# Kernel optimization log

Measured on AMD Instinct MI355X. Metric: run time of the kernel, lower is better.

Reference implementation:

```python
import jax, jax.numpy as jnp
import numpy as np

H = 768  # bert-base hidden size; match MLP width = 2*H = 1536


def setup_inputs() -> dict:
    key = jax.random.key(0)
    ks = jax.random.split(key, 6)
    B, S = 2, 256
    std = 0.02  # TruncatedNormal(stddev=initializer_range)
    return {
        "hidden": jax.random.normal(ks[0], (B, S, H), dtype=jnp.float32),
        "w_start": jax.random.normal(ks[1], (H, 1), dtype=jnp.float32) * std,
        "b_start": jnp.zeros((1,), jnp.float32),
        "w_end": jax.random.normal(ks[2], (H, 1), dtype=jnp.float32) * std,
        "b_end": jnp.zeros((1,), jnp.float32),
        "w1": jax.random.normal(ks[3], (2 * H, 2 * H), dtype=jnp.float32) * std,
        "b1": jnp.zeros((2 * H,), jnp.float32),
        "w2": jax.random.normal(ks[4], (2 * H, 1), dtype=jnp.float32) * std,
        "b2": jnp.zeros((1,), jnp.float32),
    }


def reference(hidden, w_start, b_start, w_end, b_end, w1, b1, w2, b2):
    # hidden: [B, S, H] = BERT sequence output (dropout disabled at inference)
    start_logits = hidden @ w_start + b_start  # [B, S, 1]
    end_logits = hidden @ w_end + b_end        # [B, S, 1]

    # Pairwise span features: concat(row_i, col_j) along last dim, fed to dense1.
    # concat([row, col]) @ w1 == row @ w1[:H] + col @ w1[H:], so we split w1 and
    # broadcast-add instead of materializing the [B,S,S,2H] concat tile.
    row_proj = hidden @ w1[:H]   # [B, S, 2H] (start-token contribution)
    col_proj = hidden @ w1[H:]   # [B, S, 2H] (end-token contribution)
    pre = row_proj[:, :, None, :] + col_proj[:, None, :, :] + b1  # [B, S, S, 2H]
    act = jax.nn.gelu(pre, approximate=False)  # keras 'gelu' is exact
    match_logits = act @ w2 + b2  # [B, S, S, 1]
    return start_logits, end_logits, match_logits
```

## Files before the change

kernel.cpp:

```cpp
#include <hip/hip_runtime.h>
#include <stdint.h>

typedef __attribute__((ext_vector_type(8))) __bf16 bf16x8;
typedef __attribute__((ext_vector_type(4))) float  floatx4;
typedef __attribute__((ext_vector_type(4))) unsigned int uint4v;
typedef __attribute__((ext_vector_type(2))) unsigned int uint2v;
typedef __attribute__((ext_vector_type(4))) float  float4v;
typedef __attribute__((ext_vector_type(2))) float  float2v;

__device__ __forceinline__ unsigned short f2bf(float f) {
  union { float f; unsigned int u; } x; x.f = f;
  unsigned int r = x.u + 0x7fffu + ((x.u >> 16) & 1u);
  return (unsigned short)(r >> 16);
}

__global__ __launch_bounds__(256) void logits_init_kernel(
    const float* __restrict__ hidden, const float* __restrict__ w_start,
    const float* __restrict__ b_start, const float* __restrict__ w_end,
    const float* __restrict__ b_end, const float* __restrict__ b2,
    float* __restrict__ out) {
  if (blockIdx.x >= 32) {
    float v = b2[0];
    int idx = ((blockIdx.x - 32) * 256 + threadIdx.x) * 4;
    *(float4v*)(out + 1024 + idx) = float4v{v, v, v, v};
    return;
  }
  const int tid  = threadIdx.x;
  const int lane = tid & 63;
  const int wv   = tid >> 6;
  const int wg   = blockIdx.x * 4 + wv;

  float wsv[12], wev[12];
#pragma unroll
  for (int t = 0; t < 12; ++t) {
    wsv[t] = w_start[lane + 64 * t];
    wev[t] = w_end[lane + 64 * t];
  }
  const float bs = b_start[0];
  const float be = b_end[0];

#pragma unroll
  for (int r = 0; r < 4; ++r) {
    int row = wg * 4 + r;
    const float* h = hidden + (size_t)row * 768;
    float ps = 0.f, pe = 0.f;
#pragma unroll
    for (int t = 0; t < 12; ++t) {
      float hv = h[lane + 64 * t];
      ps += hv * wsv[t];
      pe += hv * wev[t];
    }
#pragma unroll
    for (int off = 32; off >= 1; off >>= 1) {
      ps += __shfl_xor(ps, off, 64);
      pe += __shfl_xor(pe, off, 64);
    }
    if (lane == 0) { out[row] = ps + bs; out[512 + row] = pe + be; }
  }
}

__global__ __launch_bounds__(256) void proj_kernel(
    const float* __restrict__ hidden, const float* __restrict__ w1,
    const float* __restrict__ b1, unsigned short* __restrict__ wsR,
    unsigned short* __restrict__ wsC) {
  __shared__ short As[4 * 32 * 8];
  __shared__ short Bs[4 * 64 * 8];

  const int tid  = threadIdx.x;
  const int lane = tid & 63;
  const int wave = tid >> 6;
  const int wr = wave >> 1, wc = wave & 1;
  const int m0 = blockIdx.y * 32;
  const int n0g = blockIdx.x * 64;
  const bool isR = (n0g < 1536);
  const int kbase = isR ? 0 : 768;
  const int n0 = isR ? n0g : (n0g - 1536);
  const int q = lane >> 4, l15 = lane & 15;

  floatx4 acc0 = {}, acc1 = {};

  const int a_row = tid >> 3;
  const int a_s   = tid & 7;
  const int b_n   = tid & 63;
  const int b_kg  = tid >> 6;

  const float* hrow = hidden + (size_t)(m0 + a_row) * 768 + a_s * 4;
  const float* bcol = w1 + (size_t)(kbase + b_kg * 8) * 1536 + n0 + b_n;

  float4v hv = *(const float4v*)(hrow);
  float bv[8];
#pragma unroll
  for (int a = 0; a < 8; ++a) bv[a] = bcol[(size_t)a * 1536];

  const int aq = a_s >> 1;
  const int aj = (a_s & 1) * 4;

  for (int ko = 0; ko < 768; ko += 32) {
    uint2v au;
    au[0] = (unsigned int)f2bf(hv[0]) | ((unsigned int)f2bf(hv[1]) << 16);
    au[1] = (unsigned int)f2bf(hv[2]) | ((unsigned int)f2bf(hv[3]) << 16);
    *(uint2v*)(&As[(aq * 32 + a_row) * 8 + aj]) = au;
    uint4v pv;
#pragma unroll
    for (int a = 0; a < 4; ++a) {
      unsigned int lo = f2bf(bv[2 * a]);
      unsigned int hi = f2bf(bv[2 * a + 1]);
      pv[a] = lo | (hi << 16);
    }
    *(uint4v*)(&Bs[(b_kg * 64 + b_n) * 8]) = pv;
    __syncthreads();

    if (ko + 32 < 768) {
      hv = *(const float4v*)(hrow + ko + 32);
      const float* bp = bcol + (size_t)(ko + 32) * 1536;
#pragma unroll
      for (int a = 0; a < 8; ++a) bv[a] = bp[(size_t)a * 1536];
    }

    bf16x8 af  = *(const bf16x8*)(&As[(q * 32 + 16 * wr + l15) * 8]);
    bf16x8 bg0 = *(const bf16x8*)(&Bs[(q * 64 + 32 * wc + l15) * 8]);
    bf16x8 bg1 = *(const bf16x8*)(&Bs[(q * 64 + 32 * wc + 16 + l15) * 8]);
    acc0 = __builtin_amdgcn_mfma_f32_16x16x32_bf16(af, bg0, acc0, 0, 0, 0);
    acc1 = __builtin_amdgcn_mfma_f32_16x16x32_bf16(af, bg1, acc1, 0, 0, 0);
    __syncthreads();
  }

  unsigned short* outp = isR ? wsR : wsC;
#pragma unroll
  for (int ni = 0; ni < 2; ++ni) {
    const floatx4& ac = ni ? acc1 : acc0;
    int col = n0 + 32 * wc + 16 * ni + l15;
    float bias = isR ? b1[col] : 0.0f;
#pragma unroll
    for (int r = 0; r < 4; ++r) {
      int rowg = m0 + 16 * wr + q * 4 + r;
      outp[(size_t)rowg * 1536 + col] = f2bf(ac[r] + bias);
    }
  }
}

__device__ __forceinline__ float2v gelu2_acc(float2v x, float2v wv, float2v acc) {
  constexpr float C0 = 0.39103831f;
  constexpr float C1 = -0.05415410f;
  constexpr float C2 = 0.00461682f;
  constexpr float C3 = -1.51033e-4f;
  float2v xc;
  xc[0] = __builtin_amdgcn_fmed3f(x[0], -3.5f, 3.5f);
  xc[1] = __builtin_amdgcn_fmed3f(x[1], -3.5f, 3.5f);
  float2v u = xc * xc;
  float2v p = __builtin_elementwise_fma(u,
      __builtin_elementwise_fma(u,
          __builtin_elementwise_fma(u, float2v{C3, C3}, float2v{C2, C2}),
          float2v{C1, C1}),
      float2v{C0, C0});
  float2v t = __builtin_elementwise_fma(xc, p, float2v{0.5f, 0.5f});
  float2v g = x * t;
  return __builtin_elementwise_fma(g, wv, acc);
}

__device__ __forceinline__ void g8(float2v& acc, float4v r0, float4v r1,
                                   float4v c0, float4v c1,
                                   float4v w0, float4v w1) {
  acc = gelu2_acc(float2v{r0[0], r0[1]} + float2v{c0[0], c0[1]},
                  float2v{w0[0], w0[1]}, acc);
  acc = gelu2_acc(float2v{r0[2], r0[3]} + float2v{c0[2], c0[3]},
                  float2v{w0[2], w0[3]}, acc);
  acc = gelu2_acc(float2v{r1[0], r1[1]} + float2v{c1[0], c1[1]},
                  float2v{w1[0], w1[1]}, acc);
  acc = gelu2_acc(float2v{r1[2], r1[3]} + float2v{c1[2], c1[3]},
                  float2v{w1[2], w1[3]}, acc);
}

__device__ __forceinline__ void cvt8(uint4v v, float4v& lo4, float4v& hi4) {
  union { unsigned int u; float f; } t;
  float4v L, H;
  t.u = v[0] << 16;          L[0] = t.f;
  t.u = v[0] & 0xffff0000u;  L[1] = t.f;
  t.u = v[1] << 16;          L[2] = t.f;
  t.u = v[1] & 0xffff0000u;  L[3] = t.f;
  t.u = v[2] << 16;          H[0] = t.f;
  t.u = v[2] & 0xffff0000u;  H[1] = t.f;
  t.u = v[3] << 16;          H[2] = t.f;
  t.u = v[3] & 0xffff0000u;  H[3] = t.f;
  lo4 = L; hi4 = H;
}

__global__ __launch_bounds__(256) void match_kernel(
    const unsigned short* __restrict__ wsR,
    const unsigned short* __restrict__ wsC,
    const float* __restrict__ w2,
    float* __restrict__ outm) {
  __shared__ float Rs[32 * 132];
  __shared__ float Cs[64 * 132];
  __shared__ float Ws[128];

  const int tid = threadIdx.x;
  const int jt = blockIdx.x;
  const int it = blockIdx.y;
  const int bz = blockIdx.z >> 2;
  const int kh = blockIdx.z & 3;

  const int rg  = tid >> 4;
  const int cgl = tid & 15;

  float2v accA0 = {}, accA1 = {}, accA2 = {}, accA3 = {};
  float2v accB0 = {}, accB1 = {}, accB2 = {}, accB3 = {};

  const int srow = tid >> 4;
  const int sseg = tid & 15;

  const float* rp0 = &Rs[(2 * rg + 0) * 132];
  const float* rp1 = &Rs[(2 * rg + 1) * 132];
  const float* cp0 = &Cs[(cgl +  0) * 132];
  const float* cp1 = &Cs[(cgl + 16) * 132];
  const float* cp2 = &Cs[(cgl + 32) * 132];
  const float* cp3 = &Cs[(cgl + 48) * 132];

  for (int kc = 0; kc < 3; ++kc) {
    const int Kb = kh * 384 + kc * 128;
#pragma unroll
    for (int a = 0; a < 2; ++a) {
      int row = srow + 16 * a;
      const unsigned short* g =
          wsR + (size_t)(bz * 256 + it * 32 + row) * 1536 + Kb + sseg * 8;
      uint4v v = *(const uint4v*)g;
      float4v lo, hi; cvt8(v, lo, hi);
      float* d = &Rs[row * 132 + sseg * 8];
      *(float4v*)d = lo;
      *(float4v*)(d + 4) = hi;
    }
#pragma unroll
    for (int a = 0; a < 4; ++a) {
      int row = srow + 16 * a;
      const unsigned short* g =
          wsC + (size_t)(bz * 256 + jt * 64 + row) * 1536 + Kb + sseg * 8;
      uint4v v = *(const uint4v*)g;
      float4v lo, hi; cvt8(v, lo, hi);
      float* d = &Cs[row * 132 + sseg * 8];
      *(float4v*)d = lo;
      *(float4v*)(d + 4) = hi;
    }
    if (tid < 128) Ws[tid] = w2[Kb + tid];
    __syncthreads();

#pragma unroll 2
    for (int k = 0; k < 128; k += 8) {
      float4v ra0 = *(const float4v*)(rp0 + k);
      float4v ra1 = *(const float4v*)(rp0 + k + 4);
      float4v rb0 = *(const float4v*)(rp1 + k);
      float4v rb1 = *(const float4v*)(rp1 + k + 4);
      float4v w0  = *(const float4v*)(&Ws[k]);
      float4v w1  = *(const float4v*)(&Ws[k + 4]);
      {
        float4v c0 = *(const float4v*)(cp0 + k);
        float4v c1 = *(const float4v*)(cp0 + k + 4);
        g8(accA0, ra0, ra1, c0, c1, w0, w1);
        g8(accB0, rb0, rb1, c0, c1, w0, w1);
      }
      {
        float4v c0 = *(const float4v*)(cp1 + k);
        float4v c1 = *(const float4v*)(cp1 + k + 4);
        g8(accA1, ra0, ra1, c0, c1, w0, w1);
        g8(accB1, rb0, rb1, c0, c1, w0, w1);
      }
      {
        float4v c0 = *(const float4v*)(cp2 + k);
        float4v c1 = *(const float4v*)(cp2 + k + 4);
        g8(accA2, ra0, ra1, c0, c1, w0, w1);
        g8(accB2, rb0, rb1, c0, c1, w0, w1);
      }
      {
        float4v c0 = *(const float4v*)(cp3 + k);
        float4v c1 = *(const float4v*)(cp3 + k + 4);
        g8(accA3, ra0, ra1, c0, c1, w0, w1);
        g8(accB3, rb0, rb1, c0, c1, w0, w1);
      }
    }
    __syncthreads();
  }

  const size_t rowA = (size_t)(bz * 256 + it * 32 + 2 * rg);
  const size_t base = rowA * 256 + jt * 64 + cgl;
  unsafeAtomicAdd(&outm[base +  0], accA0[0] + accA0[1]);
  unsafeAtomicAdd(&outm[base + 16], accA1[0] + accA1[1]);
  unsafeAtomicAdd(&outm[base + 32], accA2[0] + accA2[1]);
  unsafeAtomicAdd(&outm[base + 48], accA3[0] + accA3[1]);
  unsafeAtomicAdd(&outm[base + 256 +  0], accB0[0] + accB0[1]);
  unsafeAtomicAdd(&outm[base + 256 + 16], accB1[0] + accB1[1]);
  unsafeAtomicAdd(&outm[base + 256 + 32], accB2[0] + accB2[1]);
  unsafeAtomicAdd(&outm[base + 256 + 48], accB3[0] + accB3[1]);
}

extern "C" void kernel_launch(void* const* d_in, const int* in_sizes, int n_in,
                              void* d_out, int out_size, void* d_ws, size_t ws_size,
                              hipStream_t stream) {
  const float* hidden  = (const float*)d_in[0];
  const float* w_start = (const float*)d_in[1];
  const float* b_start = (const float*)d_in[2];
  const float* w_end   = (const float*)d_in[3];
  const float* b_end   = (const float*)d_in[4];
  const float* w1      = (const float*)d_in[5];
  const float* b1      = (const float*)d_in[6];
  const float* w2      = (const float*)d_in[7];
  const float* b2      = (const float*)d_in[8];

  float* out = (float*)d_out;
  char* ws = (char*)d_ws;
  unsigned short* wsR = (unsigned short*)(ws);
  unsigned short* wsC = (unsigned short*)(ws + 1572864);

  logits_init_kernel<<<dim3(160), dim3(256), 0, stream>>>(
      hidden, w_start, b_start, w_end, b_end, b2, out);
  proj_kernel<<<dim3(48, 16), dim3(256), 0, stream>>>(hidden, w1, b1, wsR, wsC);
  match_kernel<<<dim3(4, 8, 8), dim3(256), 0, stream>>>(wsR, wsC, w2, out + 1024);
}
```

Measured before the change: 147.3 us.

## Split match kernel K across more blocks and force packed f32 GELU ops

Doubles the K-split of the match kernel from 4 to 8 slices (grid z 8→16), halving each block's K chunk to 64 and shrinking shared tiles. This doubles the block count (256→512) for better occupancy and smaller LDS per block. It also replaces vector-builtin GELU arithmetic with inline-asm v_pk_add/mul/fma_f32 so two lanes are processed per instruction. The cost is more atomic/partial writes to the output and inline asm that may hinder compiler scheduling.

```diff
diff --git a/kernel.cpp b/kernel.cpp
--- a/kernel.cpp
+++ b/kernel.cpp
@@ -139,36 +139,51 @@
   }
 }
 
-__device__ __forceinline__ float2v gelu2_acc(float2v x, float2v wv, float2v acc) {
-  constexpr float C0 = 0.39103831f;
-  constexpr float C1 = -0.05415410f;
-  constexpr float C2 = 0.00461682f;
-  constexpr float C3 = -1.51033e-4f;
+__device__ __forceinline__ float2v pk_add(float2v a, float2v b) {
+  float2v d;
+  asm("v_pk_add_f32 %0, %1, %2" : "=v"(d) : "v"(a), "v"(b));
+  return d;
+}
+__device__ __forceinline__ float2v pk_mul(float2v a, float2v b) {
+  float2v d;
+  asm("v_pk_mul_f32 %0, %1, %2" : "=v"(d) : "v"(a), "v"(b));
+  return d;
+}
+__device__ __forceinline__ float2v pk_fma(float2v a, float2v b, float2v c) {
+  float2v d;
+  asm("v_pk_fma_f32 %0, %1, %2, %3" : "=v"(d) : "v"(a), "v"(b), "v"(c));
+  return d;
+}
+
+__device__ __forceinline__ void gelu2_acc(float2v& acc, float2v r, float2v c,
+                                          float2v wv) {
+  const float2v C0v = {0.39103831f, 0.39103831f};
+  const float2v C1v = {-0.05415410f, -0.05415410f};
+  const float2v C2v = {0.00461682f, 0.00461682f};
+  const float2v C3v = {-1.51033e-4f, -1.51033e-4f};
+  const float2v H = {0.5f, 0.5f};
+  float2v x = pk_add(r, c);
   float2v xc;
   xc[0] = __builtin_amdgcn_fmed3f(x[0], -3.5f, 3.5f);
   xc[1] = __builtin_amdgcn_fmed3f(x[1], -3.5f, 3.5f);
-  float2v u = xc * xc;
-  float2v p = __builtin_elementwise_fma(u,
-      __builtin_elementwise_fma(u,
-          __builtin_elementwise_fma(u, float2v{C3, C3}, float2v{C2, C2}),
-          float2v{C1, C1}),
-      float2v{C0, C0});
-  float2v t = __builtin_elementwise_fma(xc, p, float2v{0.5f, 0.5f});
-  float2v g = x * t;
-  return __builtin_elementwise_fma(g, wv, acc);
+  float2v u = pk_mul(xc, xc);
+  float2v p = pk_fma(u, pk_fma(u, pk_fma(u, C3v, C2v), C1v), C0v);
+  float2v t = pk_fma(xc, p, H);
+  float2v g = pk_mul(x, t);
+  acc = pk_fma(g, wv, acc);
 }
 
 __device__ __forceinline__ void g8(float2v& acc, float4v r0, float4v r1,
                                    float4v c0, float4v c1,
                                    float4v w0, float4v w1) {
-  acc = gelu2_acc(float2v{r0[0], r0[1]} + float2v{c0[0], c0[1]},
-                  float2v{w0[0], w0[1]}, acc);
-  acc = gelu2_acc(float2v{r0[2], r0[3]} + float2v{c0[2], c0[3]},
-                  float2v{w0[2], w0[3]}, acc);
-  acc = gelu2_acc(float2v{r1[0], r1[1]} + float2v{c1[0], c1[1]},
-                  float2v{w1[0], w1[1]}, acc);
-  acc = gelu2_acc(float2v{r1[2], r1[3]} + float2v{c1[2], c1[3]},
-                  float2v{w1[2], w1[3]}, acc);
+  gelu2_acc(acc, float2v{r0[0], r0[1]}, float2v{c0[0], c0[1]},
+            float2v{w0[0], w0[1]});
+  gelu2_acc(acc, float2v{r0[2], r0[3]}, float2v{c0[2], c0[3]},
+            float2v{w0[2], w0[3]});
+  gelu2_acc(acc, float2v{r1[0], r1[1]}, float2v{c1[0], c1[1]},
+            float2v{w1[0], w1[1]});
+  gelu2_acc(acc, float2v{r1[2], r1[3]}, float2v{c1[2], c1[3]},
+            float2v{w1[2], w1[3]});
 }
 
 __device__ __forceinline__ void cvt8(uint4v v, float4v& lo4, float4v& hi4) {
@@ -190,15 +205,15 @@
     const unsigned short* __restrict__ wsC,
     const float* __restrict__ w2,
     float* __restrict__ outm) {
-  __shared__ float Rs[32 * 132];
-  __shared__ float Cs[64 * 132];
-  __shared__ float Ws[128];
+  __shared__ float Rs[32 * 68];
+  __shared__ float Cs[64 * 68];
+  __shared__ float Ws[64];
 
   const int tid = threadIdx.x;
   const int jt = blockIdx.x;
   const int it = blockIdx.y;
-  const int bz = blockIdx.z >> 2;
-  const int kh = blockIdx.z & 3;
+  const int bz = blockIdx.z >> 3;
+  const int kh = blockIdx.z & 7;
 
   const int rg  = tid >> 4;
   const int cgl = tid & 15;
@@ -206,45 +221,43 @@
   float2v accA0 = {}, accA1 = {}, accA2 = {}, accA3 = {};
   float2v accB0 = {}, accB1 = {}, accB2 = {}, accB3 = {};
 
-  const int srow = tid >> 4;
-  const int sseg = tid & 15;
-
-  const float* rp0 = &Rs[(2 * rg + 0) * 132];
-  const float* rp1 = &Rs[(2 * rg + 1) * 132];
-  const float* cp0 = &Cs[(cgl +  0) * 132];
-  const float* cp1 = &Cs[(cgl + 16) * 132];
-  const float* cp2 = &Cs[(cgl + 32) * 132];
-  const float* cp3 = &Cs[(cgl + 48) * 132];
+  const int srow = tid >> 3;
+  const int sseg = tid & 7;
+
+  const float* rp0 = &Rs[(2 * rg + 0) * 68];
+  const float* rp1 = &Rs[(2 * rg + 1) * 68];
+  const float* cp0 = &Cs[(cgl +  0) * 68];
+  const float* cp1 = &Cs[(cgl + 16) * 68];
+  const float* cp2 = &Cs[(cgl + 32) * 68];
+  const float* cp3 = &Cs[(cgl + 48) * 68];
 
   for (int kc = 0; kc < 3; ++kc) {
-    const int Kb = kh * 384 + kc * 128;
-#pragma unroll
-    for (int a = 0; a < 2; ++a) {
-      int row = srow + 16 * a;
+    const int Kb = kh * 192 + kc * 64;
+    {
       const unsigned short* g =
-          wsR + (size_t)(bz * 256 + it * 32 + row) * 1536 + Kb + sseg * 8;
+          wsR + (size_t)(bz * 256 + it * 32 + srow) * 1536 + Kb + sseg * 8;
       uint4v v = *(const uint4v*)g;
       float4v lo, hi; cvt8(v, lo, hi);
-      float* d = &Rs[row * 132 + sseg * 8];
+      float* d = &Rs[srow * 68 + sseg * 8];
       *(float4v*)d = lo;
       *(float4v*)(d + 4) = hi;
     }
 #pragma unroll
-    for (int a = 0; a < 4; ++a) {
-      int row = srow + 16 * a;
+    for (int a = 0; a < 2; ++a) {
+      int row = srow + 32 * a;
       const unsigned short* g =
           wsC + (size_t)(bz * 256 + jt * 64 + row) * 1536 + Kb + sseg * 8;
       uint4v v = *(const uint4v*)g;
       float4v lo, hi; cvt8(v, lo, hi);
-      float* d = &Cs[row * 132 + sseg * 8];
+      float* d = &Cs[row * 68 + sseg * 8];
       *(float4v*)d = lo;
       *(float4v*)(d + 4) = hi;
     }
-    if (tid < 128) Ws[tid] = w2[Kb + tid];
+    if (tid < 64) Ws[tid] = w2[Kb + tid];
     __syncthreads();
 
 #pragma unroll 2
-    for (int k = 0; k < 128; k += 8) {
+    for (int k = 0; k < 64; k += 8) {
       float4v ra0 = *(const float4v*)(rp0 + k);
       float4v ra1 = *(const float4v*)(rp0 + k + 4);
       float4v rb0 = *(const float4v*)(rp1 + k);
@@ -312,5 +325,5 @@
   logits_init_kernel<<<dim3(160), dim3(256), 0, stream>>>(
       hidden, w_start, b_start, w_end, b_end, b2, out);
   proj_kernel<<<dim3(48, 16), dim3(256), 0, stream>>>(hidden, w1, b1, wsR, wsC);
-  match_kernel<<<dim3(4, 8, 8), dim3(256), 0, stream>>>(wsR, wsC, w2, out + 1024);
-}
+  match_kernel<<<dim3(4, 8, 16), dim3(256), 0, stream>>>(wsR, wsC, w2, out + 1024);
+}
```

After: 131.5 us. 1.12x faster.

## Evaluate GELU in packed fp16 with fdot2 and fuse logits into projection

Applied to the files above, without the earlier changes.

Converts the bf16 projections to packed fp16 in shared memory and evaluates the polynomial GELU with half2 arithmetic. Each weighted pair is accumulated with fdot2, which roughly doubles ALU throughput per instruction in the dominant match kernel. The K dimension is split 24 ways instead of 4, so there are more blocks and more atomics. The start/end logits and the output initialisation are folded into an extra row of the projection grid, removing one launch. The fp16 polynomial carries accuracy risk relative to the exact GELU.

```diff
diff --git a/kernel.cpp b/kernel.cpp
--- a/kernel.cpp
+++ b/kernel.cpp
@@ -6,7 +6,7 @@
 typedef __attribute__((ext_vector_type(4))) unsigned int uint4v;
 typedef __attribute__((ext_vector_type(2))) unsigned int uint2v;
 typedef __attribute__((ext_vector_type(4))) float  float4v;
-typedef __attribute__((ext_vector_type(2))) float  float2v;
+typedef __attribute__((ext_vector_type(2))) _Float16 half2v;
 
 __device__ __forceinline__ unsigned short f2bf(float f) {
   union { float f; unsigned int u; } x; x.f = f;
@@ -14,59 +14,59 @@
   return (unsigned short)(r >> 16);
 }
 
-__global__ __launch_bounds__(256) void logits_init_kernel(
-    const float* __restrict__ hidden, const float* __restrict__ w_start,
-    const float* __restrict__ b_start, const float* __restrict__ w_end,
-    const float* __restrict__ b_end, const float* __restrict__ b2,
-    float* __restrict__ out) {
-  if (blockIdx.x >= 32) {
-    float v = b2[0];
-    int idx = ((blockIdx.x - 32) * 256 + threadIdx.x) * 4;
-    *(float4v*)(out + 1024 + idx) = float4v{v, v, v, v};
-    return;
-  }
-  const int tid  = threadIdx.x;
-  const int lane = tid & 63;
-  const int wv   = tid >> 6;
-  const int wg   = blockIdx.x * 4 + wv;
-
-  float wsv[12], wev[12];
-#pragma unroll
-  for (int t = 0; t < 12; ++t) {
-    wsv[t] = w_start[lane + 64 * t];
-    wev[t] = w_end[lane + 64 * t];
-  }
-  const float bs = b_start[0];
-  const float be = b_end[0];
-
-#pragma unroll
-  for (int r = 0; r < 4; ++r) {
-    int row = wg * 4 + r;
-    const float* h = hidden + (size_t)row * 768;
-    float ps = 0.f, pe = 0.f;
-#pragma unroll
-    for (int t = 0; t < 12; ++t) {
-      float hv = h[lane + 64 * t];
-      ps += hv * wsv[t];
-      pe += hv * wev[t];
-    }
-#pragma unroll
-    for (int off = 32; off >= 1; off >>= 1) {
-      ps += __shfl_xor(ps, off, 64);
-      pe += __shfl_xor(pe, off, 64);
-    }
-    if (lane == 0) { out[row] = ps + bs; out[512 + row] = pe + be; }
-  }
-}
-
 __global__ __launch_bounds__(256) void proj_kernel(
     const float* __restrict__ hidden, const float* __restrict__ w1,
     const float* __restrict__ b1, unsigned short* __restrict__ wsR,
-    unsigned short* __restrict__ wsC) {
+    unsigned short* __restrict__ wsC,
+    const float* __restrict__ w_start, const float* __restrict__ b_start,
+    const float* __restrict__ w_end, const float* __restrict__ b_end,
+    const float* __restrict__ b2, float* __restrict__ out) {
+  const int tid  = threadIdx.x;
+  if (blockIdx.y == 16) {
+    if (blockIdx.x >= 32) {
+      float v = b2[0];
+      float4v vv = {v, v, v, v};
+      int base = (blockIdx.x - 32) * 8192 + tid * 4;
+#pragma unroll
+      for (int itr = 0; itr < 8; ++itr)
+        *(float4v*)(out + 1024 + base + itr * 1024) = vv;
+      return;
+    }
+    const int lane = tid & 63;
+    const int wv   = tid >> 6;
+    const int wg   = blockIdx.x * 4 + wv;
+    float wsv[12], wev[12];
+#pragma unroll
+    for (int t = 0; t < 12; ++t) {
+      wsv[t] = w_start[lane + 64 * t];
+      wev[t] = w_end[lane + 64 * t];
+    }
+    const float bs = b_start[0];
+    const float be = b_end[0];
+#pragma unroll
+    for (int r = 0; r < 4; ++r) {
+      int row = wg * 4 + r;
+      const float* h = hidden + (size_t)row * 768;
+      float ps = 0.f, pe = 0.f;
+#pragma unroll
+      for (int t = 0; t < 12; ++t) {
+        float hv = h[lane + 64 * t];
+        ps += hv * wsv[t];
+        pe += hv * wev[t];
+      }
+#pragma unroll
+      for (int off = 32; off >= 1; off >>= 1) {
+        ps += __shfl_xor(ps, off, 64);
+        pe += __shfl_xor(pe, off, 64);
+      }
+      if (lane == 0) { out[row] = ps + bs; out[512 + row] = pe + be; }
+    }
+    return;
+  }
+
   __shared__ short As[4 * 32 * 8];
   __shared__ short Bs[4 * 64 * 8];
 
-  const int tid  = threadIdx.x;
   const int lane = tid & 63;
   const int wave = tid >> 6;
   const int wr = wave >> 1, wc = wave & 1;
@@ -139,50 +139,41 @@
   }
 }
 
-__device__ __forceinline__ float2v gelu2_acc(float2v x, float2v wv, float2v acc) {
-  constexpr float C0 = 0.39103831f;
-  constexpr float C1 = -0.05415410f;
-  constexpr float C2 = 0.00461682f;
-  constexpr float C3 = -1.51033e-4f;
-  float2v xc;
-  xc[0] = __builtin_amdgcn_fmed3f(x[0], -3.5f, 3.5f);
-  xc[1] = __builtin_amdgcn_fmed3f(x[1], -3.5f, 3.5f);
-  float2v u = xc * xc;
-  float2v p = __builtin_elementwise_fma(u,
+__device__ __forceinline__ void gelu_pair(float& acc, unsigned int ru,
+                                          unsigned int cu, unsigned int wu) {
+  const half2v C3 = {(_Float16)-1.51033e-4f, (_Float16)-1.51033e-4f};
+  const half2v C2 = {(_Float16)0.00461682f, (_Float16)0.00461682f};
+  const half2v C1 = {(_Float16)-0.05415410f, (_Float16)-0.05415410f};
+  const half2v C0 = {(_Float16)0.39103831f, (_Float16)0.39103831f};
+  const half2v HI = {(_Float16)3.5f, (_Float16)3.5f};
+  const half2v LO = {(_Float16)-3.5f, (_Float16)-3.5f};
+  const half2v HALF = {(_Float16)0.5f, (_Float16)0.5f};
+  half2v r = __builtin_bit_cast(half2v, ru);
+  half2v c = __builtin_bit_cast(half2v, cu);
+  half2v w = __builtin_bit_cast(half2v, wu);
+  half2v x = r + c;
+  half2v xc = __builtin_elementwise_min(
+      __builtin_elementwise_max(x, LO), HI);
+  half2v u = xc * xc;
+  half2v p = __builtin_elementwise_fma(u,
       __builtin_elementwise_fma(u,
-          __builtin_elementwise_fma(u, float2v{C3, C3}, float2v{C2, C2}),
-          float2v{C1, C1}),
-      float2v{C0, C0});
-  float2v t = __builtin_elementwise_fma(xc, p, float2v{0.5f, 0.5f});
-  float2v g = x * t;
-  return __builtin_elementwise_fma(g, wv, acc);
-}
-
-__device__ __forceinline__ void g8(float2v& acc, float4v r0, float4v r1,
-                                   float4v c0, float4v c1,
-                                   float4v w0, float4v w1) {
-  acc = gelu2_acc(float2v{r0[0], r0[1]} + float2v{c0[0], c0[1]},
-                  float2v{w0[0], w0[1]}, acc);
-  acc = gelu2_acc(float2v{r0[2], r0[3]} + float2v{c0[2], c0[3]},
-                  float2v{w0[2], w0[3]}, acc);
-  acc = gelu2_acc(float2v{r1[0], r1[1]} + float2v{c1[0], c1[1]},
-                  float2v{w1[0], w1[1]}, acc);
-  acc = gelu2_acc(float2v{r1[2], r1[3]} + float2v{c1[2], c1[3]},
-                  float2v{w1[2], w1[3]}, acc);
-}
-
-__device__ __forceinline__ void cvt8(uint4v v, float4v& lo4, float4v& hi4) {
-  union { unsigned int u; float f; } t;
-  float4v L, H;
-  t.u = v[0] << 16;          L[0] = t.f;
-  t.u = v[0] & 0xffff0000u;  L[1] = t.f;
-  t.u = v[1] << 16;          L[2] = t.f;
-  t.u = v[1] & 0xffff0000u;  L[3] = t.f;
-  t.u = v[2] << 16;          H[0] = t.f;
-  t.u = v[2] & 0xffff0000u;  H[1] = t.f;
-  t.u = v[3] << 16;          H[2] = t.f;
-  t.u = v[3] & 0xffff0000u;  H[3] = t.f;
-  lo4 = L; hi4 = H;
+          __builtin_elementwise_fma(u, C3, C2), C1), C0);
+  half2v t = __builtin_elementwise_fma(xc, p, HALF);
+  half2v g = x * t;
+  acc = __builtin_amdgcn_fdot2(g, w, acc, false);
+}
+
+__device__ __forceinline__ uint4v bf8_to_h8(uint4v v) {
+  uint4v o;
+#pragma unroll
+  for (int a = 0; a < 4; ++a) {
+    union { unsigned int u; float f; } lo, hi;
+    lo.u = v[a] << 16;
+    hi.u = v[a] & 0xffff0000u;
+    auto h = __builtin_amdgcn_cvt_pkrtz(lo.f, hi.f);
+    o[a] = __builtin_bit_cast(unsigned int, h);
+  }
+  return o;
 }
 
 __global__ __launch_bounds__(256) void match_kernel(
@@ -190,105 +181,99 @@
     const unsigned short* __restrict__ wsC,
     const float* __restrict__ w2,
     float* __restrict__ outm) {
-  __shared__ float Rs[32 * 132];
-  __shared__ float Cs[64 * 132];
-  __shared__ float Ws[128];
+  __shared__ unsigned int RsU[32 * 36];
+  __shared__ unsigned int CsU[64 * 36];
+  __shared__ unsigned int WsU[32];
 
   const int tid = threadIdx.x;
   const int jt = blockIdx.x;
   const int it = blockIdx.y;
-  const int bz = blockIdx.z >> 2;
-  const int kh = blockIdx.z & 3;
+  const int bz = blockIdx.z / 24;
+  const int kh = blockIdx.z % 24;
+  const int Kb = kh * 64;
 
   const int rg  = tid >> 4;
   const int cgl = tid & 15;
 
-  float2v accA0 = {}, accA1 = {}, accA2 = {}, accA3 = {};
-  float2v accB0 = {}, accB1 = {}, accB2 = {}, accB3 = {};
-
-  const int srow = tid >> 4;
-  const int sseg = tid & 15;
-
-  const float* rp0 = &Rs[(2 * rg + 0) * 132];
-  const float* rp1 = &Rs[(2 * rg + 1) * 132];
-  const float* cp0 = &Cs[(cgl +  0) * 132];
-  const float* cp1 = &Cs[(cgl + 16) * 132];
-  const float* cp2 = &Cs[(cgl + 32) * 132];
-  const float* cp3 = &Cs[(cgl + 48) * 132];
-
-  for (int kc = 0; kc < 3; ++kc) {
-    const int Kb = kh * 384 + kc * 128;
-#pragma unroll
-    for (int a = 0; a < 2; ++a) {
-      int row = srow + 16 * a;
-      const unsigned short* g =
-          wsR + (size_t)(bz * 256 + it * 32 + row) * 1536 + Kb + sseg * 8;
-      uint4v v = *(const uint4v*)g;
-      float4v lo, hi; cvt8(v, lo, hi);
-      float* d = &Rs[row * 132 + sseg * 8];
-      *(float4v*)d = lo;
-      *(float4v*)(d + 4) = hi;
-    }
-#pragma unroll
-    for (int a = 0; a < 4; ++a) {
-      int row = srow + 16 * a;
-      const unsigned short* g =
-          wsC + (size_t)(bz * 256 + jt * 64 + row) * 1536 + Kb + sseg * 8;
-      uint4v v = *(const uint4v*)g;
-      float4v lo, hi; cvt8(v, lo, hi);
-      float* d = &Cs[row * 132 + sseg * 8];
-      *(float4v*)d = lo;
-      *(float4v*)(d + 4) = hi;
-    }
-    if (tid < 128) Ws[tid] = w2[Kb + tid];
-    __syncthreads();
+  float accA0 = 0.f, accA1 = 0.f, accA2 = 0.f, accA3 = 0.f;
+  float accB0 = 0.f, accB1 = 0.f, accB2 = 0.f, accB3 = 0.f;
+
+  const int srow = tid >> 3;
+  const int sseg = tid & 7;
+  {
+    const unsigned short* g =
+        wsR + (size_t)(bz * 256 + it * 32 + srow) * 1536 + Kb + sseg * 8;
+    *(uint4v*)(RsU + srow * 36 + sseg * 4) = bf8_to_h8(*(const uint4v*)g);
+  }
+#pragma unroll
+  for (int a = 0; a < 2; ++a) {
+    int row = srow + 32 * a;
+    const unsigned short* g =
+        wsC + (size_t)(bz * 256 + jt * 64 + row) * 1536 + Kb + sseg * 8;
+    *(uint4v*)(CsU + row * 36 + sseg * 4) = bf8_to_h8(*(const uint4v*)g);
+  }
+  if (tid < 32) {
+    auto h = __builtin_amdgcn_cvt_pkrtz(w2[Kb + 2 * tid], w2[Kb + 2 * tid + 1]);
+    WsU[tid] = __builtin_bit_cast(unsigned int, h);
+  }
+  __syncthreads();
+
+  const unsigned int* rap = RsU + (2 * rg + 0) * 36;
+  const unsigned int* rbp = RsU + (2 * rg + 1) * 36;
+  const unsigned int* c0p = CsU + (cgl +  0) * 36;
+  const unsigned int* c1p = CsU + (cgl + 16) * 36;
+  const unsigned int* c2p = CsU + (cgl + 32) * 36;
+  const unsigned int* c3p = CsU + (cgl + 48) * 36;
 
 #pragma unroll 2
-    for (int k = 0; k < 128; k += 8) {
-      float4v ra0 = *(const float4v*)(rp0 + k);
-      float4v ra1 = *(const float4v*)(rp0 + k + 4);
-      float4v rb0 = *(const float4v*)(rp1 + k);
-      float4v rb1 = *(const float4v*)(rp1 + k + 4);
-      float4v w0  = *(const float4v*)(&Ws[k]);
-      float4v w1  = *(const float4v*)(&Ws[k + 4]);
-      {
-        float4v c0 = *(const float4v*)(cp0 + k);
-        float4v c1 = *(const float4v*)(cp0 + k + 4);
-        g8(accA0, ra0, ra1, c0, c1, w0, w1);
-        g8(accB0, rb0, rb1, c0, c1, w0, w1);
-      }
-      {
-        float4v c0 = *(const float4v*)(cp1 + k);
-        float4v c1 = *(const float4v*)(cp1 + k + 4);
-        g8(accA1, ra0, ra1, c0, c1, w0, w1);
-        g8(accB1, rb0, rb1, c0, c1, w0, w1);
-      }
-      {
-        float4v c0 = *(const float4v*)(cp2 + k);
-        float4v c1 = *(const float4v*)(cp2 + k + 4);
-        g8(accA2, ra0, ra1, c0, c1, w0, w1);
-        g8(accB2, rb0, rb1, c0, c1, w0, w1);
-      }
-      {
-        float4v c0 = *(const float4v*)(cp3 + k);
-        float4v c1 = *(const float4v*)(cp3 + k + 4);
-        g8(accA3, ra0, ra1, c0, c1, w0, w1);
-        g8(accB3, rb0, rb1, c0, c1, w0, w1);
-      }
-    }
-    __syncthreads();
+  for (int ks = 0; ks < 8; ++ks) {
+    uint4v ra = *(const uint4v*)(rap + ks * 4);
+    uint4v rb = *(const uint4v*)(rbp + ks * 4);
+    uint4v wv = *(const uint4v*)(WsU + ks * 4);
+    {
+      uint4v cv = *(const uint4v*)(c0p + ks * 4);
+#pragma unroll
+      for (int p = 0; p < 4; ++p) {
+        gelu_pair(accA0, ra[p], cv[p], wv[p]);
+        gelu_pair(accB0, rb[p], cv[p], wv[p]);
+      }
+    }
+    {
+      uint4v cv = *(const uint4v*)(c1p + ks * 4);
+#pragma unroll
+      for (int p = 0; p < 4; ++p) {
+        gelu_pair(accA1, ra[p], cv[p], wv[p]);
+        gelu_pair(accB1, rb[p], cv[p], wv[p]);
+      }
+    }
+    {
+      uint4v cv = *(const uint4v*)(c2p + ks * 4);
+#pragma unroll
+      for (int p = 0; p < 4; ++p) {
+        gelu_pair(accA2, ra[p], cv[p], wv[p]);
+        gelu_pair(accB2, rb[p], cv[p], wv[p]);
+      }
+    }
+    {
+      uint4v cv = *(const uint4v*)(c3p + ks * 4);
+#pragma unroll
+      for (int p = 0; p < 4; ++p) {
+        gelu_pair(accA3, ra[p], cv[p], wv[p]);
+        gelu_pair(accB3, rb[p], cv[p], wv[p]);
+      }
+    }
   }
 
   const size_t rowA = (size_t)(bz * 256 + it * 32 + 2 * rg);
   const size_t base = rowA * 256 + jt * 64 + cgl;
-  unsafeAtomicAdd(&outm[base +  0], accA0[0] + accA0[1]);
-  unsafeAtomicAdd(&outm[base + 16], accA1[0] + accA1[1]);
-  unsafeAtomicAdd(&outm[base + 32], accA2[0] + accA2[1]);
-  unsafeAtomicAdd(&outm[base + 48], accA3[0] + accA3[1]);
-  unsafeAtomicAdd(&outm[base + 256 +  0], accB0[0] + accB0[1]);
-  unsafeAtomicAdd(&outm[base + 256 + 16], accB1[0] + accB1[1]);
-  unsafeAtomicAdd(&outm[base + 256 + 32], accB2[0] + accB2[1]);
-  unsafeAtomicAdd(&outm[base + 256 + 48], accB3[0] + accB3[1]);
+  unsafeAtomicAdd(&outm[base +  0], accA0);
+  unsafeAtomicAdd(&outm[base + 16], accA1);
+  unsafeAtomicAdd(&outm[base + 32], accA2);
+  unsafeAtomicAdd(&outm[base + 48], accA3);
+  unsafeAtomicAdd(&outm[base + 256 +  0], accB0);
+  unsafeAtomicAdd(&outm[base + 256 + 16], accB1);
+  unsafeAtomicAdd(&outm[base + 256 + 32], accB2);
+  unsafeAtomicAdd(&outm[base + 256 + 48], accB3);
 }
 
 extern "C" void kernel_launch(void* const* d_in, const int* in_sizes, int n_in,
@@ -309,8 +294,7 @@
   unsigned short* wsR = (unsigned short*)(ws);
   unsigned short* wsC = (unsigned short*)(ws + 1572864);
 
-  logits_init_kernel<<<dim3(160), dim3(256), 0, stream>>>(
-      hidden, w_start, b_start, w_end, b_end, b2, out);
-  proj_kernel<<<dim3(48, 16), dim3(256), 0, stream>>>(hidden, w1, b1, wsR, wsC);
-  match_kernel<<<dim3(4, 8, 8), dim3(256), 0, stream>>>(wsR, wsC, w2, out + 1024);
-}
+  proj_kernel<<<dim3(48, 17), dim3(256), 0, stream>>>(
+      hidden, w1, b1, wsR, wsC, w_start, b_start, w_end, b_end, b2, out);
+  match_kernel<<<dim3(4, 8, 48), dim3(256), 0, stream>>>(wsR, wsC, w2, out + 1024);
+}
```

New measurement: 123.6 us. 16.1% less time.
